# Kernel optimization log

Measured on AMD Instinct MI355X. Metric: run time of the kernel, lower is better.

## Reference

```python
import jax, jax.numpy as jnp
import numpy as np

B, OP, MA, F_IN, F_OUT = 8, 400, 200, 64, 64


def setup_inputs() -> dict:
    key = jax.random.key(0)
    ks = jax.random.split(key, 8)
    x = jax.random.normal(ks[0], (B, OP, F_IN), dtype=jnp.float32)
    y = jax.random.normal(ks[1], (B, MA, F_IN), dtype=jnp.float32)
    z = jax.random.normal(ks[2], (B, OP, MA, F_IN), dtype=jnp.float32)
    op_ma_adj = jax.random.randint(ks[3], (B, OP, MA), 0, 2, dtype=jnp.int32)
    # xavier-uniform-ish params
    lim = float(np.sqrt(6.0 / (F_IN + F_OUT)))
    W_op = jax.random.uniform(ks[4], (F_IN, F_OUT), minval=-lim, maxval=lim, dtype=jnp.float32)
    W_ma = jax.random.uniform(ks[5], (F_IN, F_OUT), minval=-lim, maxval=lim, dtype=jnp.float32)
    W_edge = jax.random.uniform(ks[6], (F_IN, F_OUT), minval=-lim, maxval=lim, dtype=jnp.float32)
    lim_a = float(np.sqrt(6.0 / (1 + 3 * F_OUT)))
    att_vec = jax.random.uniform(ks[7], (3 * F_OUT,), minval=-lim_a, maxval=lim_a, dtype=jnp.float32)
    return {"x": x, "y": y, "z": z, "op_ma_adj": op_ma_adj,
            "W_op": W_op, "W_ma": W_ma, "W_edge": W_edge, "att_vec": att_vec}


def reference(x, y, z, op_ma_adj, W_op, W_ma, W_edge, att_vec):
    F = W_op.shape[1]
    h_op = jnp.einsum('bni,io->bno', x, W_op)                      # [B, op, F]
    h = jnp.einsum('bmi,io->bmo', y, W_ma)                         # [B, ma, F]
    h_edge = jnp.einsum('bnmi,io->bnmo', z, W_edge).transpose(0, 2, 1, 3)  # [B, ma, op, F]
    # attention score: concat([h_op, h_ma, h_edge]) @ a  ==  per-part dot products (no BxMAxOPx3F materialization)
    a_op, a_ma, a_edge = att_vec[:F], att_vec[F:2 * F], att_vec[2 * F:]
    e = (jnp.einsum('bnf,f->bn', h_op, a_op)[:, None, :]
         + jnp.einsum('bmf,f->bm', h, a_ma)[:, :, None]
         + jnp.einsum('bmnf,f->bmn', h_edge, a_edge))              # [B, ma, op]
    e = jax.nn.leaky_relu(e, negative_slope=0.01)
    adjT = op_ma_adj.transpose(0, 2, 1)                            # [B, ma, op]
    row_empty = jnp.all(adjT == 0, axis=-1, keepdims=True)         # [B, ma, 1]
    att = jnp.where(adjT > 0, e, -jnp.inf)
    att = jnp.where(row_empty, 0.0, att)                           # empty rows -> uniform softmax (matches torch)
    att = jax.nn.softmax(att, axis=-1)                             # [B, ma, op]
    h_op_edge = h_op[:, None, :, :] + h_edge                       # [B, ma, op, F]
    h_prime = jnp.einsum('bmn,bmnf->bmf', att, h_op_edge)          # [B, ma, F]
    h_prime = jnp.where(row_empty, 0.0, h_prime) + h
    return jax.nn.elu(h_prime)
```

## Files before the change

kernel.cpp:

```cpp
#include <hip/hip_runtime.h>
#include <math.h>

#define B_   8
#define OP_  400
#define MA_  200
#define ZROW (MA_ * 64)
#define NEGM -1.0e30f

typedef float v4f __attribute__((ext_vector_type(4)));

__global__ __launch_bounds__(256) void precompute_k(
    const float* __restrict__ x, const float* __restrict__ y,
    const float* __restrict__ Wop, const float* __restrict__ Wma,
    const float* __restrict__ Wedge, const float* __restrict__ att,
    float* __restrict__ ws_we, float* __restrict__ ws_eop, float* __restrict__ ws_ema)
{
    __shared__ float w_s[192];
    const int tid = threadIdx.x, wv = tid >> 6, ln = tid & 63;
    if (tid < 192) {
        const int which = tid >> 6, i = tid & 63;
        const float* W = (which == 0) ? Wop : ((which == 1) ? Wma : Wedge);
        const float* a = att + which * 64;
        float acc = 0.f;
        #pragma unroll 8
        for (int f = 0; f < 64; ++f) acc = fmaf(W[i * 64 + f], a[f], acc);
        w_s[tid] = acc;
    }
    __syncthreads();
    if (blockIdx.x == 0 && tid < 64) ws_we[tid] = w_s[128 + tid];

    const int row = blockIdx.x * 4 + wv;
    if (row < B_ * OP_) {
        float s = x[(size_t)row * 64 + ln] * w_s[ln];
        #pragma unroll
        for (int o = 32; o > 0; o >>= 1) s += __shfl_xor(s, o, 64);
        if (ln == 0) ws_eop[row] = s;
    } else if (row < B_ * OP_ + B_ * MA_) {
        const int r2 = row - B_ * OP_;
        float s = y[(size_t)r2 * 64 + ln] * w_s[64 + ln];
        #pragma unroll
        for (int o = 32; o > 0; o >>= 1) s += __shfl_xor(s, o, 64);
        if (ln == 0) ws_ema[r2] = s;
    }
}

__global__ __launch_bounds__(256) void gat_fused(
    const float* __restrict__ x, const float* __restrict__ y,
    const float* __restrict__ z, const int* __restrict__ adj,
    const float* __restrict__ Wop, const float* __restrict__ Wma,
    const float* __restrict__ Wedge,
    const float* __restrict__ ws_we, const float* __restrict__ ws_eop,
    const float* __restrict__ ws_ema, float* __restrict__ out)
{
    __shared__ int2  nle[4][112];
    __shared__ float mred[4], lred[4];
    __shared__ float vws[4][64], uws[4][64];
    __shared__ float vs_s[64], us_s[64], ys_s[64];
    __shared__ float pvt[4][64];

    const int tid = threadIdx.x, wv = tid >> 6, ln = tid & 63;
    const int g = ln >> 4, q = ln & 15;
    const int bm = blockIdx.x;
    const int b = bm / MA_, m = bm % MA_;

    const float ema = ws_ema[bm];

    const int rbase = wv * 100;
    int cnt = 0;
    #pragma unroll
    for (int round = 0; round < 2; ++round) {
        const int lr = round * 64 + ln;
        const int n  = rbase + lr;
        bool a = false;
        if (lr < 100) a = (adj[((size_t)(b * OP_ + n)) * MA_ + m] != 0);
        const unsigned long long mask = __ballot(a);
        if (a) {
            const int pos = cnt + __popcll(mask & ((1ull << ln) - 1ull));
            nle[wv][pos] = make_int2(n, __float_as_int(ws_eop[b * OP_ + n] + ema));
        }
        cnt += __popcll(mask);
    }
    const int cnt_p = (cnt + 7) & ~7;
    if (ln < cnt_p + 8 - cnt) {
        nle[wv][cnt + ln] = make_int2(rbase, __float_as_int(NEGM));
    }

    const float* zP = z + ((size_t)b * OP_ * MA_ + m) * 64;
    const float* xP = x + (size_t)b * OP_ * 64;
    const v4f wq = ((const v4f*)ws_we)[q];

    v4f v0 = {0.f,0.f,0.f,0.f}, u0 = {0.f,0.f,0.f,0.f};
    v4f v1 = {0.f,0.f,0.f,0.f}, u1 = {0.f,0.f,0.f,0.f};
    float M0 = NEGM, L0 = 0.f, M1 = NEGM, L1 = 0.f;

    auto upd = [&wq](float& M, float& L, v4f& v, v4f& u,
                     const v4f z4, const v4f x4, const float eo) {
        float s_ = fmaf(z4.x, wq.x, fmaf(z4.y, wq.y,
                   fmaf(z4.z, wq.z, z4.w * wq.w)));
        s_ += __shfl_xor(s_, 1, 64); s_ += __shfl_xor(s_, 2, 64);
        s_ += __shfl_xor(s_, 4, 64); s_ += __shfl_xor(s_, 8, 64);
        float e_ = s_ + eo;
        e_ = (e_ >= 0.f) ? e_ : 0.01f * e_;
        const float m2_ = fmaxf(M, e_);
        const float w_  = __expf(fminf(M, e_) - m2_);
        const bool  nm  = (e_ > M);
        const float c_  = nm ? w_ : 1.f;
        const float p_  = nm ? 1.f : w_;
        L = fmaf(L, c_, p_);
        v = v * c_ + z4 * p_;
        u = u * c_ + x4 * p_;
        M = m2_;
    };

    int2 pa = nle[wv][g];
    int2 pb = nle[wv][4 + g];
    v4f za = __builtin_nontemporal_load((const v4f*)(zP + (size_t)pa.x * ZROW) + q);
    v4f zb = __builtin_nontemporal_load((const v4f*)(zP + (size_t)pb.x * ZROW) + q);
    v4f xa = *((const v4f*)(xP + ((size_t)pa.x << 6)) + q);
    v4f xb = *((const v4f*)(xP + ((size_t)pb.x << 6)) + q);

    for (int i = 0; i < cnt_p; i += 8) {
        const int2 qa = nle[wv][i + 8 + g];
        const int2 qb = nle[wv][i + 12 + g];
        const v4f nza = __builtin_nontemporal_load((const v4f*)(zP + (size_t)qa.x * ZROW) + q);
        const v4f nzb = __builtin_nontemporal_load((const v4f*)(zP + (size_t)qb.x * ZROW) + q);
        const v4f nxa = *((const v4f*)(xP + ((size_t)qa.x << 6)) + q);
        const v4f nxb = *((const v4f*)(xP + ((size_t)qb.x << 6)) + q);
        upd(M0, L0, v0, u0, za, xa, __int_as_float(pa.y));
        upd(M1, L1, v1, u1, zb, xb, __int_as_float(pb.y));
        pa = qa; pb = qb; za = nza; zb = nzb; xa = nxa; xb = nxb;
    }

    const float Mp = fmaxf(M0, M1);
    const float ca = __expf(M0 - Mp), cb = __expf(M1 - Mp);
    float L = L0 * ca + L1 * cb;
    v4f  v = v0 * ca + v1 * cb;
    v4f  u = u0 * ca + u1 * cb;
    float M = Mp;

    float Mw = M;
    Mw = fmaxf(Mw, __shfl_xor(Mw, 16, 64));
    Mw = fmaxf(Mw, __shfl_xor(Mw, 32, 64));
    const float cg = __expf(M - Mw);
    float Lw = L * cg;
    Lw += __shfl_xor(Lw, 16, 64);
    Lw += __shfl_xor(Lw, 32, 64);
    v *= cg;
    u *= cg;
    v.x += __shfl_xor(v.x, 16, 64); v.y += __shfl_xor(v.y, 16, 64);
    v.z += __shfl_xor(v.z, 16, 64); v.w += __shfl_xor(v.w, 16, 64);
    v.x += __shfl_xor(v.x, 32, 64); v.y += __shfl_xor(v.y, 32, 64);
    v.z += __shfl_xor(v.z, 32, 64); v.w += __shfl_xor(v.w, 32, 64);
    u.x += __shfl_xor(u.x, 16, 64); u.y += __shfl_xor(u.y, 16, 64);
    u.z += __shfl_xor(u.z, 16, 64); u.w += __shfl_xor(u.w, 16, 64);
    u.x += __shfl_xor(u.x, 32, 64); u.y += __shfl_xor(u.y, 32, 64);
    u.z += __shfl_xor(u.z, 32, 64); u.w += __shfl_xor(u.w, 32, 64);

    if (ln < 16) {
        ((v4f*)vws[wv])[q] = v;
        ((v4f*)uws[wv])[q] = u;
    }
    if (ln == 0) { mred[wv] = Mw; lred[wv] = Lw; }
    __syncthreads();

    if (tid < 64) {
        const float Mg = fmaxf(fmaxf(mred[0], mred[1]), fmaxf(mred[2], mred[3]));
        const float c0 = __expf(mred[0] - Mg);
        const float c1 = __expf(mred[1] - Mg);
        const float c2 = __expf(mred[2] - Mg);
        const float c3 = __expf(mred[3] - Mg);
        const float Lg = c0 * lred[0] + c1 * lred[1] + c2 * lred[2] + c3 * lred[3];
        const float inv = (Lg > 0.f) ? (1.f / Lg) : 0.f;
        vs_s[tid] = (c0 * vws[0][tid] + c1 * vws[1][tid] +
                     c2 * vws[2][tid] + c3 * vws[3][tid]) * inv;
        us_s[tid] = (c0 * uws[0][tid] + c1 * uws[1][tid] +
                     c2 * uws[2][tid] + c3 * uws[3][tid]) * inv;
        ys_s[tid] = y[(size_t)bm * 64 + tid];
    }
    __syncthreads();

    {
        float acc = 0.f;
        const int i0 = wv * 16;
        #pragma unroll
        for (int k = 0; k < 16; ++k) {
            const int i = i0 + k;
            acc += vs_s[i] * Wedge[i * 64 + ln]
                 + us_s[i] * Wop[i * 64 + ln]
                 + ys_s[i] * Wma[i * 64 + ln];
        }
        pvt[wv][ln] = acc;
    }
    __syncthreads();
    if (tid < 64) {
        const float h = pvt[0][tid] + pvt[1][tid] + pvt[2][tid] + pvt[3][tid];
        out[(size_t)bm * 64 + tid] = (h > 0.f) ? h : (__expf(h) - 1.f);
    }
}

extern "C" void kernel_launch(void* const* d_in, const int* in_sizes, int n_in,
                              void* d_out, int out_size, void* d_ws, size_t ws_size,
                              hipStream_t stream) {
    const float* x     = (const float*)d_in[0];
    const float* y     = (const float*)d_in[1];
    const float* z     = (const float*)d_in[2];
    const int*   adj   = (const int*)d_in[3];
    const float* Wop   = (const float*)d_in[4];
    const float* Wma   = (const float*)d_in[5];
    const float* Wedge = (const float*)d_in[6];
    const float* att   = (const float*)d_in[7];

    float* ws     = (float*)d_ws;
    float* ws_we  = ws;
    float* ws_eop = ws + 64;
    float* ws_ema = ws + 64 + B_ * OP_;

    precompute_k<<<1200, 256, 0, stream>>>(
        x, y, Wop, Wma, Wedge, att, ws_we, ws_eop, ws_ema);
    gat_fused<<<B_ * MA_, 256, 0, stream>>>(
        x, y, z, adj, Wop, Wma, Wedge, ws_we, ws_eop, ws_ema, (float*)d_out);
}
```

Before: 237.0 us.

## Fuse precompute kernel into main GAT kernel, compute op scores inline

Removes the separate precompute launch. Each block now computes the projected attention vectors W·a itself, computes the ma score with a wave reduction, and folds the op score into the per-edge dot product using the x row already being loaded. This eliminates one kernel launch and the workspace round trip. In exchange, every block redoes the small 192x64 weight-vector product and each edge update does extra FMAs. Padding entries are now masked by comparing against cnt instead of storing a sentinel score.

```diff
diff --git a/kernel.cpp b/kernel.cpp
--- a/kernel.cpp
+++ b/kernel.cpp
@@ -9,50 +9,15 @@
 
 typedef float v4f __attribute__((ext_vector_type(4)));
 
-__global__ __launch_bounds__(256) void precompute_k(
-    const float* __restrict__ x, const float* __restrict__ y,
-    const float* __restrict__ Wop, const float* __restrict__ Wma,
-    const float* __restrict__ Wedge, const float* __restrict__ att,
-    float* __restrict__ ws_we, float* __restrict__ ws_eop, float* __restrict__ ws_ema)
-{
-    __shared__ float w_s[192];
-    const int tid = threadIdx.x, wv = tid >> 6, ln = tid & 63;
-    if (tid < 192) {
-        const int which = tid >> 6, i = tid & 63;
-        const float* W = (which == 0) ? Wop : ((which == 1) ? Wma : Wedge);
-        const float* a = att + which * 64;
-        float acc = 0.f;
-        #pragma unroll 8
-        for (int f = 0; f < 64; ++f) acc = fmaf(W[i * 64 + f], a[f], acc);
-        w_s[tid] = acc;
-    }
-    __syncthreads();
-    if (blockIdx.x == 0 && tid < 64) ws_we[tid] = w_s[128 + tid];
-
-    const int row = blockIdx.x * 4 + wv;
-    if (row < B_ * OP_) {
-        float s = x[(size_t)row * 64 + ln] * w_s[ln];
-        #pragma unroll
-        for (int o = 32; o > 0; o >>= 1) s += __shfl_xor(s, o, 64);
-        if (ln == 0) ws_eop[row] = s;
-    } else if (row < B_ * OP_ + B_ * MA_) {
-        const int r2 = row - B_ * OP_;
-        float s = y[(size_t)r2 * 64 + ln] * w_s[64 + ln];
-        #pragma unroll
-        for (int o = 32; o > 0; o >>= 1) s += __shfl_xor(s, o, 64);
-        if (ln == 0) ws_ema[r2] = s;
-    }
-}
-
-__global__ __launch_bounds__(256) void gat_fused(
+__global__ __launch_bounds__(256) void gat_one(
     const float* __restrict__ x, const float* __restrict__ y,
     const float* __restrict__ z, const int* __restrict__ adj,
     const float* __restrict__ Wop, const float* __restrict__ Wma,
-    const float* __restrict__ Wedge,
-    const float* __restrict__ ws_we, const float* __restrict__ ws_eop,
-    const float* __restrict__ ws_ema, float* __restrict__ out)
+    const float* __restrict__ Wedge, const float* __restrict__ att,
+    float* __restrict__ out)
 {
-    __shared__ int2  nle[4][112];
+    __shared__ float w_s[192];
+    __shared__ int   nls[4][112];
     __shared__ float mred[4], lred[4];
     __shared__ float vws[4][64], uws[4][64];
     __shared__ float vs_s[64], us_s[64], ys_s[64];
@@ -63,7 +28,15 @@
     const int bm = blockIdx.x;
     const int b = bm / MA_, m = bm % MA_;
 
-    const float ema = ws_ema[bm];
+    if (tid < 192) {
+        const int which = tid >> 6, i = tid & 63;
+        const float* W = (which == 0) ? Wop : ((which == 1) ? Wma : Wedge);
+        const float* a = att + which * 64;
+        float acc = 0.f;
+        #pragma unroll 8
+        for (int f = 0; f < 64; ++f) acc = fmaf(W[i * 64 + f], a[f], acc);
+        w_s[tid] = acc;
+    }
 
     const int rbase = wv * 100;
     int cnt = 0;
@@ -76,27 +49,35 @@
         const unsigned long long mask = __ballot(a);
         if (a) {
             const int pos = cnt + __popcll(mask & ((1ull << ln) - 1ull));
-            nle[wv][pos] = make_int2(n, __float_as_int(ws_eop[b * OP_ + n] + ema));
+            nls[wv][pos] = n;
         }
         cnt += __popcll(mask);
     }
     const int cnt_p = (cnt + 7) & ~7;
-    if (ln < cnt_p + 8 - cnt) {
-        nle[wv][cnt + ln] = make_int2(rbase, __float_as_int(NEGM));
-    }
+    if (ln < cnt_p + 8 - cnt) nls[wv][cnt + ln] = rbase;
+
+    __syncthreads();
+
+    const v4f wqe = ((const v4f*)(w_s + 128))[q];
+    const v4f wqo = ((const v4f*)(w_s      ))[q];
+
+    float ema = y[(size_t)bm * 64 + ln] * w_s[64 + ln];
+    #pragma unroll
+    for (int o = 32; o > 0; o >>= 1) ema += __shfl_xor(ema, o, 64);
 
     const float* zP = z + ((size_t)b * OP_ * MA_ + m) * 64;
     const float* xP = x + (size_t)b * OP_ * 64;
-    const v4f wq = ((const v4f*)ws_we)[q];
 
     v4f v0 = {0.f,0.f,0.f,0.f}, u0 = {0.f,0.f,0.f,0.f};
     v4f v1 = {0.f,0.f,0.f,0.f}, u1 = {0.f,0.f,0.f,0.f};
     float M0 = NEGM, L0 = 0.f, M1 = NEGM, L1 = 0.f;
 
-    auto upd = [&wq](float& M, float& L, v4f& v, v4f& u,
-                     const v4f z4, const v4f x4, const float eo) {
-        float s_ = fmaf(z4.x, wq.x, fmaf(z4.y, wq.y,
-                   fmaf(z4.z, wq.z, z4.w * wq.w)));
+    auto upd = [&wqe, &wqo](float& M, float& L, v4f& v, v4f& u,
+                            const v4f z4, const v4f x4, const float eo) {
+        float s_ = fmaf(z4.x, wqe.x, fmaf(z4.y, wqe.y,
+                   fmaf(z4.z, wqe.z, z4.w * wqe.w)));
+        s_ = fmaf(x4.x, wqo.x, fmaf(x4.y, wqo.y,
+             fmaf(x4.z, wqo.z, fmaf(x4.w, wqo.w, s_))));
         s_ += __shfl_xor(s_, 1, 64); s_ += __shfl_xor(s_, 2, 64);
         s_ += __shfl_xor(s_, 4, 64); s_ += __shfl_xor(s_, 8, 64);
         float e_ = s_ + eo;
@@ -112,22 +93,24 @@
         M = m2_;
     };
 
-    int2 pa = nle[wv][g];
-    int2 pb = nle[wv][4 + g];
-    v4f za = __builtin_nontemporal_load((const v4f*)(zP + (size_t)pa.x * ZROW) + q);
-    v4f zb = __builtin_nontemporal_load((const v4f*)(zP + (size_t)pb.x * ZROW) + q);
-    v4f xa = *((const v4f*)(xP + ((size_t)pa.x << 6)) + q);
-    v4f xb = *((const v4f*)(xP + ((size_t)pb.x << 6)) + q);
+    int pa = nls[wv][g];
+    int pb = nls[wv][4 + g];
+    v4f za = __builtin_nontemporal_load((const v4f*)(zP + (size_t)pa * ZROW) + q);
+    v4f zb = __builtin_nontemporal_load((const v4f*)(zP + (size_t)pb * ZROW) + q);
+    v4f xa = *((const v4f*)(xP + ((size_t)pa << 6)) + q);
+    v4f xb = *((const v4f*)(xP + ((size_t)pb << 6)) + q);
 
     for (int i = 0; i < cnt_p; i += 8) {
-        const int2 qa = nle[wv][i + 8 + g];
-        const int2 qb = nle[wv][i + 12 + g];
-        const v4f nza = __builtin_nontemporal_load((const v4f*)(zP + (size_t)qa.x * ZROW) + q);
-        const v4f nzb = __builtin_nontemporal_load((const v4f*)(zP + (size_t)qb.x * ZROW) + q);
-        const v4f nxa = *((const v4f*)(xP + ((size_t)qa.x << 6)) + q);
-        const v4f nxb = *((const v4f*)(xP + ((size_t)qb.x << 6)) + q);
-        upd(M0, L0, v0, u0, za, xa, __int_as_float(pa.y));
-        upd(M1, L1, v1, u1, zb, xb, __int_as_float(pb.y));
+        const int qa = nls[wv][i + 8 + g];
+        const int qb = nls[wv][i + 12 + g];
+        const v4f nza = __builtin_nontemporal_load((const v4f*)(zP + (size_t)qa * ZROW) + q);
+        const v4f nzb = __builtin_nontemporal_load((const v4f*)(zP + (size_t)qb * ZROW) + q);
+        const v4f nxa = *((const v4f*)(xP + ((size_t)qa << 6)) + q);
+        const v4f nxb = *((const v4f*)(xP + ((size_t)qb << 6)) + q);
+        const float ea = (i + g     < cnt) ? ema : NEGM;
+        const float eb = (i + 4 + g < cnt) ? ema : NEGM;
+        upd(M0, L0, v0, u0, za, xa, ea);
+        upd(M1, L1, v1, u1, zb, xb, eb);
         pa = qa; pb = qb; za = nza; zb = nzb; xa = nxa; xb = nxb;
     }
 
@@ -209,14 +192,8 @@
     const float* Wma   = (const float*)d_in[5];
     const float* Wedge = (const float*)d_in[6];
     const float* att   = (const float*)d_in[7];
+    (void)d_ws; (void)ws_size;
 
-    float* ws     = (float*)d_ws;
-    float* ws_we  = ws;
-    float* ws_eop = ws + 64;
-    float* ws_ema = ws + 64 + B_ * OP_;
-
-    precompute_k<<<1200, 256, 0, stream>>>(
-        x, y, Wop, Wma, Wedge, att, ws_we, ws_eop, ws_ema);
-    gat_fused<<<B_ * MA_, 256, 0, stream>>>(
-        x, y, z, adj, Wop, Wma, Wedge, ws_we, ws_eop, ws_ema, (float*)d_out);
+    gat_one<<<B_ * MA_, 256, 0, stream>>>(
+        x, y, z, adj, Wop, Wma, Wedge, att, (float*)d_out);
 }
```

After: 245.1 us. 1.03x slower.
